# Kernel optimization log

Hardware: AMD Instinct MI355X
Metric: run time of the kernel (lower is better)

Reference implementation:

```python
import jax, jax.numpy as jnp
import numpy as np


def setup_inputs() -> dict:
    key = jax.random.key(0)
    k1, k2, k3 = jax.random.split(key, 3)
    B, C, H, W = 32, 768, 24, 24
    feat1 = jax.random.normal(k1, (B, C, H, W), dtype=jnp.float32)
    feat2 = jax.random.normal(k2, (B, C, H, W), dtype=jnp.float32)
    gamma = jax.random.normal(k3, (1,), dtype=jnp.float32)
    return {"feat1": feat1, "feat2": feat2, "gamma": gamma}


def reference(feat1, feat2, gamma):
    # CMA: channel-wise cross-modal attention over flattened spatial dim.
    B, C, H, W = feat1.shape
    q = feat1.reshape(B, C, H * W)          # [B, C, HW]
    kv = feat2.reshape(B, C, H * W)         # [B, C, HW] (k and v share this)
    attn = jnp.einsum('bcn,bdn->bcd', q, kv)          # [B, C, C] = q @ k^T
    attn = jax.nn.softmax(attn, axis=-1)
    info = jnp.einsum('bcd,bdn->bcn', attn, kv)       # [B, C, HW]
    info = info.reshape(B, C, H, W)
    return gamma[0] * info + feat1
```

## Files before the change

kernel.cpp:

```cpp
#include <hip/hip_runtime.h>

#define B_  32
#define C_  768
#define HW_ 576

#define NCQ 18
#define NCP 24

typedef _Float16 half8 __attribute__((ext_vector_type(8)));
typedef _Float16 half4 __attribute__((ext_vector_type(4)));
typedef float    f32x4 __attribute__((ext_vector_type(4)));

__device__ __forceinline__ void g2l16(const void* g, void* l) {
    __builtin_amdgcn_global_load_lds(
        (const __attribute__((address_space(1))) unsigned int*)g,
        (__attribute__((address_space(3))) unsigned int*)l, 16, 0, 0);
}

__device__ __forceinline__ int xcd_swz(int orig, int nwg) {
    int q = nwg >> 3, rr = nwg & 7;
    int xcd = orig & 7, idx = orig >> 3;
    int base = (xcd < rr) ? xcd * (q + 1) : rr * (q + 1) + (xcd - rr) * q;
    return base + idx;
}

__global__ __launch_bounds__(256) void prep_all(const float* __restrict__ f1,
                                                const float* __restrict__ f2,
                                                char* __restrict__ q16,
                                                char* __restrict__ kv16,
                                                char* __restrict__ vt,
                                                int b0, int nqk) {
    const int bid = blockIdx.x;
    if (bid < nqk) {
        int idx = bid * 256 + threadIdx.x;
        int x   = idx & 3;
        int row = (idx >> 2) & 127;
        int t3  = idx >> 9;
        int k0  = t3 % 18;
        int t4  = t3 / 18;
        int ti  = t4 % 6;
        int bz  = t4 / 6;
        int kc  = x ^ ((row >> 1) & 3);
        size_t src = ((size_t)(b0 + bz) * C_ + ti * 128 + row) * HW_ + k0 * 32 + kc * 8;
        f32x4 a0 = *(const f32x4*)(f1 + src);
        f32x4 a1 = *(const f32x4*)(f1 + src + 4);
        f32x4 c0 = *(const f32x4*)(f2 + src);
        f32x4 c1 = *(const f32x4*)(f2 + src + 4);
        half8 ha, hb;
        #pragma unroll
        for (int e = 0; e < 4; ++e) {
            ha[e] = (_Float16)a0[e]; ha[4 + e] = (_Float16)a1[e];
            hb[e] = (_Float16)c0[e]; hb[4 + e] = (_Float16)c1[e];
        }
        *(half8*)(q16  + (size_t)idx * 16) = ha;
        *(half8*)(kv16 + (size_t)idx * 16) = hb;
    } else {
        int idx = (bid - nqk) * 256 + threadIdx.x;
        int bz  = idx / 55296;
        int wl  = idx % 55296;
        int tj  = wl / 18432;
        int r   = wl % 18432;
        int k0  = r / 768;
        int r2  = r % 768;
        int n   = r2 >> 2;
        int x   = r2 & 3;
        int kc  = x ^ ((n >> 1) & 3);
        int c0  = k0 * 32 + kc * 8;
        const float* s = f2 + ((size_t)(b0 + bz) * C_ + c0) * HW_ + tj * 192 + n;
        half8 h;
        #pragma unroll
        for (int j = 0; j < 8; ++j) h[j] = (_Float16)s[(size_t)j * HW_];
        *(half8*)(vt + ((size_t)(bz * 3 + tj) * NCP + k0) * 12288 + n * 64 + x * 16) = h;
    }
}

__global__ __launch_bounds__(512, 4) void qk6(const char* __restrict__ q16,
                                              const char* __restrict__ kv16,
                                              float* __restrict__ attn,
                                              int nwg) {
    __shared__ __align__(16) char S[3][24576];
    const int wg = xcd_swz(blockIdx.x, nwg);
    const int bz = wg >> 4, rr0 = wg & 15, ti = rr0 >> 2, tj = rr0 & 3;
    const int t = threadIdx.x, lane = t & 63, w = t >> 6;
    const int rsub = lane >> 2, cb = (lane & 3) * 16;

    const char *p0, *p1, *p2;
    int o0, o1, o2;
    {
        auto arow = [&](int l) {
            int gr = ti * 192 + 16 * l + rsub;
            return q16 + ((size_t)(bz * 6 + (gr >> 7)) * NCQ) * 8192 + (gr & 127) * 64 + cb;
        };
        auto brow = [&](int l) {
            int gd = tj * 192 + 16 * l + rsub;
            return kv16 + ((size_t)(bz * 6 + (gd >> 7)) * NCQ) * 8192 + (gd & 127) * 64 + cb;
        };
        if (w < 4) {
            p0 = arow(2 * w);     o0 = (2 * w) * 1024;
            p1 = arow(2 * w + 1); o1 = (2 * w + 1) * 1024;
            p2 = brow(8 + w);     o2 = 12288 + (8 + w) * 1024;
        } else {
            int v = w - 4;
            p0 = brow(2 * v);     o0 = 12288 + (2 * v) * 1024;
            p1 = brow(2 * v + 1); o1 = 12288 + (2 * v + 1) * 1024;
            p2 = arow(8 + v);     o2 = (8 + v) * 1024;
        }
    }

    const int wr = (w >> 1) * 48, wc = (w & 1) * 96;
    const int r16 = lane & 15, cg = lane >> 4;
    int offA[3], offB[6];
    #pragma unroll
    for (int m = 0; m < 3; ++m) {
        int ra = wr + m * 16 + r16;
        offA[m] = ra * 64 + ((cg ^ ((ra >> 1) & 3)) << 4);
    }
    #pragma unroll
    for (int n = 0; n < 6; ++n) {
        int rb = wc + n * 16 + r16;
        offB[n] = 12288 + rb * 64 + ((cg ^ ((rb >> 1) & 3)) << 4);
    }

    f32x4 acc[3][6] = {};

#define STG(SLOT) do {                          \
        char* sb_ = &S[SLOT][0];                \
        g2l16(p0, sb_ + o0);                    \
        g2l16(p1, sb_ + o1);                    \
        g2l16(p2, sb_ + o2);                    \
        p0 += 8192; p1 += 8192; p2 += 8192;     \
    } while (0)

    STG(0); STG(1);
    int rd = 0, st = 2;
    for (int c = 0; c < NCQ; ++c) {
        if (c + 2 < NCQ) {
            STG(st); st = (st == 2) ? 0 : st + 1;
            asm volatile("s_waitcnt vmcnt(6)" ::: "memory");
        } else if (c + 2 == NCQ) {
            asm volatile("s_waitcnt vmcnt(3)" ::: "memory");
        } else {
            asm volatile("s_waitcnt vmcnt(0)" ::: "memory");
        }
        __builtin_amdgcn_s_barrier();
        const char* sb = &S[rd][0];
        rd = (rd == 2) ? 0 : rd + 1;
        half8 a0 = *(const half8*)(sb + offA[0]);
        half8 a1 = *(const half8*)(sb + offA[1]);
        half8 a2 = *(const half8*)(sb + offA[2]);
        __builtin_amdgcn_s_setprio(1);
        #pragma unroll
        for (int n = 0; n < 6; ++n) {
            half8 bn = *(const half8*)(sb + offB[n]);
            acc[0][n] = __builtin_amdgcn_mfma_f32_16x16x32_f16(a0, bn, acc[0][n], 0, 0, 0);
            acc[1][n] = __builtin_amdgcn_mfma_f32_16x16x32_f16(a1, bn, acc[1][n], 0, 0, 0);
            acc[2][n] = __builtin_amdgcn_mfma_f32_16x16x32_f16(a2, bn, acc[2][n], 0, 0, 0);
        }
        __builtin_amdgcn_s_setprio(0);
        __builtin_amdgcn_s_barrier();
    }
#undef STG

    float* ab = attn + ((size_t)bz * C_ + ti * 192) * C_ + tj * 192;
    const int col = lane & 15, rbase = (lane >> 4) * 4;
    #pragma unroll
    for (int m = 0; m < 3; ++m)
        #pragma unroll
        for (int n = 0; n < 6; ++n)
            #pragma unroll
            for (int rg = 0; rg < 4; ++rg)
                ab[(size_t)(wr + m * 16 + rbase + rg) * C_ + wc + n * 16 + col] = acc[m][n][rg];
}

__global__ __launch_bounds__(256) void softmax_p16(const float* __restrict__ attn,
                                                   char* __restrict__ p16,
                                                   const float* __restrict__ gamma) {
    const int R    = blockIdx.x * 4 + (threadIdx.x >> 6);
    const int lane = threadIdx.x & 63;
    const int bz   = R / C_;
    const int c    = R - bz * C_;
    const float* p = attn + (size_t)R * C_;

    f32x4 v[3];
    float mx = -1e30f;
    #pragma unroll
    for (int u = 0; u < 3; ++u) {
        v[u] = *(const f32x4*)(p + (size_t)(lane + 64 * u) * 4);
        #pragma unroll
        for (int e = 0; e < 4; ++e) mx = fmaxf(mx, v[u][e]);
    }
    #pragma unroll
    for (int o = 32; o > 0; o >>= 1) mx = fmaxf(mx, __shfl_xor(mx, o));

    float s = 0.f;
    #pragma unroll
    for (int u = 0; u < 3; ++u)
        #pragma unroll
        for (int e = 0; e < 4; ++e) {
            v[u][e] = __expf(v[u][e] - mx);
            s += v[u][e];
        }
    #pragma unroll
    for (int o = 32; o > 0; o >>= 1) s += __shfl_xor(s, o);
    const float scale = gamma[0] / s;

    const int sw = (c >> 1) & 3;
    char* tb = p16 + ((size_t)(bz * 6 + (c >> 7)) * NCP) * 8192;
    #pragma unroll
    for (int u = 0; u < 3; ++u) {
        int d0 = 4 * lane + 256 * u;
        int k0 = d0 >> 5;
        int x  = ((d0 >> 3) & 3) ^ sw;
        char* addr = tb + (size_t)k0 * 8192 + (c & 127) * 64 + x * 16 + (d0 & 7) * 2;
        half4 hv;
        #pragma unroll
        for (int e = 0; e < 4; ++e) hv[e] = (_Float16)(v[u][e] * scale);
        *(half4*)addr = hv;
    }
}

__global__ __launch_bounds__(512, 4) void pv6(const char* __restrict__ p16,
                                              const char* __restrict__ vt,
                                              const float* __restrict__ f1,
                                              float* __restrict__ out,
                                              int b0, int nwg) {
    __shared__ __align__(16) char S[3][24576];
    const int wg = xcd_swz(blockIdx.x, nwg);
    const int bz = wg / 12, rr0 = wg % 12, ti = rr0 / 3, tj = rr0 % 3;
    const int t = threadIdx.x, lane = t & 63, w = t >> 6;
    const int rsub = lane >> 2, cb = (lane & 3) * 16;

    const char *p0, *p1, *p2;
    int o0, o1, o2;
    long s0, s1, s2;
    {
        auto prow = [&](int l) {
            int gr = ti * 192 + 16 * l + rsub;
            return p16 + ((size_t)(bz * 6 + (gr >> 7)) * NCP) * 8192 + (gr & 127) * 64 + cb;
        };
        auto vrow = [&](int l) {
            int gn = 16 * l + rsub;
            return vt + ((size_t)(bz * 3 + tj) * NCP) * 12288 + gn * 64 + cb;
        };
        if (w < 4) {
            p0 = prow(2 * w);     o0 = (2 * w) * 1024;     s0 = 8192;
            p1 = prow(2 * w + 1); o1 = (2 * w + 1) * 1024; s1 = 8192;
            p2 = vrow(8 + w);     o2 = 12288 + (8 + w) * 1024; s2 = 12288;
        } else {
            int v = w - 4;
            p0 = vrow(2 * v);     o0 = 12288 + (2 * v) * 1024;     s0 = 12288;
            p1 = vrow(2 * v + 1); o1 = 12288 + (2 * v + 1) * 1024; s1 = 12288;
            p2 = prow(8 + v);     o2 = (8 + v) * 1024;             s2 = 8192;
        }
    }

    const int wr = (w >> 1) * 48, wc = (w & 1) * 96;
    const int r16 = lane & 15, cg = lane >> 4;
    int offA[3], offB[6];
    #pragma unroll
    for (int m = 0; m < 3; ++m) {
        int ra = wr + m * 16 + r16;
        offA[m] = ra * 64 + ((cg ^ ((ra >> 1) & 3)) << 4);
    }
    #pragma unroll
    for (int n = 0; n < 6; ++n) {
        int rb = wc + n * 16 + r16;
        offB[n] = 12288 + rb * 64 + ((cg ^ ((rb >> 1) & 3)) << 4);
    }

    f32x4 acc[3][6] = {};

#define STG(SLOT) do {                          \
        char* sb_ = &S[SLOT][0];                \
        g2l16(p0, sb_ + o0);                    \
        g2l16(p1, sb_ + o1);                    \
        g2l16(p2, sb_ + o2);                    \
        p0 += s0; p1 += s1; p2 += s2;           \
    } while (0)

    STG(0); STG(1);
    int rd = 0, st = 2;
    for (int c = 0; c < NCP; ++c) {
        if (c + 2 < NCP) {
            STG(st); st = (st == 2) ? 0 : st + 1;
            asm volatile("s_waitcnt vmcnt(6)" ::: "memory");
        } else if (c + 2 == NCP) {
            asm volatile("s_waitcnt vmcnt(3)" ::: "memory");
        } else {
            asm volatile("s_waitcnt vmcnt(0)" ::: "memory");
        }
        __builtin_amdgcn_s_barrier();
        const char* sb = &S[rd][0];
        rd = (rd == 2) ? 0 : rd + 1;
        half8 a0 = *(const half8*)(sb + offA[0]);
        half8 a1 = *(const half8*)(sb + offA[1]);
        half8 a2 = *(const half8*)(sb + offA[2]);
        __builtin_amdgcn_s_setprio(1);
        #pragma unroll
        for (int n = 0; n < 6; ++n) {
            half8 bn = *(const half8*)(sb + offB[n]);
            acc[0][n] = __builtin_amdgcn_mfma_f32_16x16x32_f16(a0, bn, acc[0][n], 0, 0, 0);
            acc[1][n] = __builtin_amdgcn_mfma_f32_16x16x32_f16(a1, bn, acc[1][n], 0, 0, 0);
            acc[2][n] = __builtin_amdgcn_mfma_f32_16x16x32_f16(a2, bn, acc[2][n], 0, 0, 0);
        }
        __builtin_amdgcn_s_setprio(0);
        __builtin_amdgcn_s_barrier();
    }
#undef STG

    const int b = b0 + bz;
    const float* f1b = f1 + ((size_t)b * C_ + ti * 192) * HW_ + tj * 192;
    float*       ob  = out + ((size_t)b * C_ + ti * 192) * HW_ + tj * 192;
    const int col = lane & 15, rbase = (lane >> 4) * 4;
    #pragma unroll
    for (int m = 0; m < 3; ++m)
        #pragma unroll
        for (int n = 0; n < 6; ++n)
            #pragma unroll
            for (int rg = 0; rg < 4; ++rg) {
                int r2 = wr + m * 16 + rbase + rg;
                int c2 = wc + n * 16 + col;
                ob[(size_t)r2 * HW_ + c2] = acc[m][n][rg] + f1b[(size_t)r2 * HW_ + c2];
            }
}

extern "C" void kernel_launch(void* const* d_in, const int* in_sizes, int n_in,
                              void* d_out, int out_size, void* d_ws, size_t ws_size,
                              hipStream_t stream) {
    const float* feat1 = (const float*)d_in[0];
    const float* feat2 = (const float*)d_in[1];
    const float* gamma = (const float*)d_in[2];
    float* out = (float*)d_out;

    const size_t SZ_Q    = (size_t)C_ * HW_ * 2;
    const size_t SZ_ATTN = (size_t)C_ * C_  * 4;
    const size_t SZ_P    = (size_t)C_ * C_  * 2;
    const size_t per_batch = SZ_ATTN + 3 * SZ_Q + SZ_P;

    int nb = (int)(ws_size / per_batch);
    if (nb < 1) nb = 1;
    if (nb > B_) nb = B_;

    char* ws    = (char*)d_ws;
    float* attn = (float*)ws;
    char* q16   = ws + (size_t)nb * SZ_ATTN;
    char* kv16  = q16 + (size_t)nb * SZ_Q;
    char* vtb   = kv16 + (size_t)nb * SZ_Q;
    char* p16   = vtb + (size_t)nb * SZ_Q;

    for (int b0 = 0; b0 < B_; b0 += nb) {
        int cur = (B_ - b0 < nb) ? (B_ - b0) : nb;
        prep_all<<<cur * 432, 256, 0, stream>>>(feat1, feat2, q16, kv16, vtb, b0, cur * 216);
        qk6<<<cur * 16, 512, 0, stream>>>(q16, kv16, attn, cur * 16);
        softmax_p16<<<cur * 192, 256, 0, stream>>>(attn, p16, gamma);
        pv6<<<cur * 12, 512, 0, stream>>>(p16, vtb, feat1, out, b0, cur * 12);
    }
}
```

Baseline: 146.5 us.

## Transpose V via shared memory and retile PV into 128x192 double-buffered tiles

The V-transpose part of prep now stages a 32x192 fp32 tile in padded shared memory, so global reads are coalesced float4 loads instead of strided scalar reads. Each block now handles one tile, which cuts the grid for that part. The PV kernel changes from 512-thread 192x192 tiles with triple buffering to 256-thread 128x192 tiles with double buffering, giving more workgroups (18 per batch) and higher occupancy. The trade-offs are shallower prefetch and more B-tile reloads across row tiles.

```diff
diff --git a/kernel.cpp b/kernel.cpp
--- a/kernel.cpp
+++ b/kernel.cpp
@@ -30,6 +30,7 @@
                                                 char* __restrict__ kv16,
                                                 char* __restrict__ vt,
                                                 int b0, int nqk) {
+    __shared__ float Vsh[32 * 201];
     const int bid = blockIdx.x;
     if (bid < nqk) {
         int idx = bid * 256 + threadIdx.x;
@@ -55,22 +56,30 @@
         *(half8*)(q16  + (size_t)idx * 16) = ha;
         *(half8*)(kv16 + (size_t)idx * 16) = hb;
     } else {
-        int idx = (bid - nqk) * 256 + threadIdx.x;
-        int bz  = idx / 55296;
-        int wl  = idx % 55296;
-        int tj  = wl / 18432;
-        int r   = wl % 18432;
-        int k0  = r / 768;
-        int r2  = r % 768;
-        int n   = r2 >> 2;
-        int x   = r2 & 3;
-        int kc  = x ^ ((n >> 1) & 3);
-        int c0  = k0 * 32 + kc * 8;
-        const float* s = f2 + ((size_t)(b0 + bz) * C_ + c0) * HW_ + tj * 192 + n;
-        half8 h;
-        #pragma unroll
-        for (int j = 0; j < 8; ++j) h[j] = (_Float16)s[(size_t)j * HW_];
-        *(half8*)(vt + ((size_t)(bz * 3 + tj) * NCP + k0) * 12288 + n * 64 + x * 16) = h;
+        int bid2 = bid - nqk;
+        int bz = bid2 / 72, rem = bid2 % 72, k0 = rem / 3, tj = rem % 3;
+        int b  = b0 + bz;
+        int t  = threadIdx.x;
+        #pragma unroll
+        for (int p = 0; p < 6; ++p) {
+            int fidx = p * 256 + t;
+            int dd = fidx / 48, c4 = fidx % 48;
+            f32x4 v = *(const f32x4*)(f2 + ((size_t)b * C_ + k0 * 32 + dd) * HW_ + tj * 192 + c4 * 4);
+            #pragma unroll
+            for (int e = 0; e < 4; ++e) Vsh[dd * 201 + c4 * 4 + e] = v[e];
+        }
+        __syncthreads();
+        char* ob = vt + ((size_t)(bz * 3 + tj) * NCP + k0) * 12288;
+        #pragma unroll
+        for (int p = 0; p < 3; ++p) {
+            int o = p * 256 + t;
+            int x = o & 3, n = o >> 2;
+            int kc = x ^ ((n >> 1) & 3);
+            half8 h;
+            #pragma unroll
+            for (int j = 0; j < 8; ++j) h[j] = (_Float16)Vsh[(kc * 8 + j) * 201 + n];
+            *(half8*)(ob + o * 16) = h;
+        }
     }
 }
 
@@ -219,106 +228,112 @@
     }
 }
 
-__global__ __launch_bounds__(512, 4) void pv6(const char* __restrict__ p16,
+__global__ __launch_bounds__(256, 8) void pv7(const char* __restrict__ p16,
                                               const char* __restrict__ vt,
                                               const float* __restrict__ f1,
                                               float* __restrict__ out,
                                               int b0, int nwg) {
-    __shared__ __align__(16) char S[3][24576];
+    __shared__ __align__(16) char S[2][20480];
     const int wg = xcd_swz(blockIdx.x, nwg);
-    const int bz = wg / 12, rr0 = wg % 12, ti = rr0 / 3, tj = rr0 % 3;
+    const int bz = wg / 18, rem = wg % 18, ti = rem / 3, tj = rem % 3;
     const int t = threadIdx.x, lane = t & 63, w = t >> 6;
     const int rsub = lane >> 2, cb = (lane & 3) * 16;
 
-    const char *p0, *p1, *p2;
-    int o0, o1, o2;
-    long s0, s1, s2;
-    {
-        auto prow = [&](int l) {
-            int gr = ti * 192 + 16 * l + rsub;
-            return p16 + ((size_t)(bz * 6 + (gr >> 7)) * NCP) * 8192 + (gr & 127) * 64 + cb;
-        };
-        auto vrow = [&](int l) {
-            int gn = 16 * l + rsub;
-            return vt + ((size_t)(bz * 3 + tj) * NCP) * 12288 + gn * 64 + cb;
-        };
-        if (w < 4) {
-            p0 = prow(2 * w);     o0 = (2 * w) * 1024;     s0 = 8192;
-            p1 = prow(2 * w + 1); o1 = (2 * w + 1) * 1024; s1 = 8192;
-            p2 = vrow(8 + w);     o2 = 12288 + (8 + w) * 1024; s2 = 12288;
-        } else {
-            int v = w - 4;
-            p0 = vrow(2 * v);     o0 = 12288 + (2 * v) * 1024;     s0 = 12288;
-            p1 = vrow(2 * v + 1); o1 = 12288 + (2 * v + 1) * 1024; s1 = 12288;
-            p2 = prow(8 + v);     o2 = (8 + v) * 1024;             s2 = 8192;
-        }
-    }
-
-    const int wr = (w >> 1) * 48, wc = (w & 1) * 96;
+    const char* Ab = p16 + ((size_t)(bz * 6 + ti) * NCP) * 8192  + rsub * 64 + cb;
+    const char* Bb = vt  + ((size_t)(bz * 3 + tj) * NCP) * 12288 + rsub * 64 + cb;
+
+    const char *p0, *p1, *p2, *p3, *p4;
+    int o0, o1, o2, o3, o4;
+    long s0, s1, s2, s3, s4;
+    if (w == 0) {
+        p0 = Ab;          o0 = 0;          s0 = 8192;
+        p1 = Ab + 1024;   o1 = 1024;       s1 = 8192;
+        p2 = Ab + 2048;   o2 = 2048;       s2 = 8192;
+        p3 = Ab + 3072;   o3 = 3072;       s3 = 8192;
+        p4 = Ab + 4096;   o4 = 4096;       s4 = 8192;
+    } else if (w == 1) {
+        p0 = Ab + 5120;   o0 = 5120;       s0 = 8192;
+        p1 = Ab + 6144;   o1 = 6144;       s1 = 8192;
+        p2 = Ab + 7168;   o2 = 7168;       s2 = 8192;
+        p3 = Bb;          o3 = 8192;       s3 = 12288;
+        p4 = Bb + 1024;   o4 = 9216;       s4 = 12288;
+    } else if (w == 2) {
+        p0 = Bb + 2048;   o0 = 10240;      s0 = 12288;
+        p1 = Bb + 3072;   o1 = 11264;      s1 = 12288;
+        p2 = Bb + 4096;   o2 = 12288;      s2 = 12288;
+        p3 = Bb + 5120;   o3 = 13312;      s3 = 12288;
+        p4 = Bb + 6144;   o4 = 14336;      s4 = 12288;
+    } else {
+        p0 = Bb + 7168;   o0 = 15360;      s0 = 12288;
+        p1 = Bb + 8192;   o1 = 16384;      s1 = 12288;
+        p2 = Bb + 9216;   o2 = 17408;      s2 = 12288;
+        p3 = Bb + 10240;  o3 = 18432;      s3 = 12288;
+        p4 = Bb + 11264;  o4 = 19456;      s4 = 12288;
+    }
+
+    const int wc = w * 48;
     const int r16 = lane & 15, cg = lane >> 4;
-    int offA[3], offB[6];
-    #pragma unroll
-    for (int m = 0; m < 3; ++m) {
-        int ra = wr + m * 16 + r16;
+    int offA[8], offB[3];
+    #pragma unroll
+    for (int m = 0; m < 8; ++m) {
+        int ra = m * 16 + r16;
         offA[m] = ra * 64 + ((cg ^ ((ra >> 1) & 3)) << 4);
     }
     #pragma unroll
-    for (int n = 0; n < 6; ++n) {
+    for (int n = 0; n < 3; ++n) {
         int rb = wc + n * 16 + r16;
-        offB[n] = 12288 + rb * 64 + ((cg ^ ((rb >> 1) & 3)) << 4);
-    }
-
-    f32x4 acc[3][6] = {};
+        offB[n] = 8192 + rb * 64 + ((cg ^ ((rb >> 1) & 3)) << 4);
+    }
+
+    f32x4 acc[8][3] = {};
 
 #define STG(SLOT) do {                          \
         char* sb_ = &S[SLOT][0];                \
-        g2l16(p0, sb_ + o0);                    \
-        g2l16(p1, sb_ + o1);                    \
-        g2l16(p2, sb_ + o2);                    \
-        p0 += s0; p1 += s1; p2 += s2;           \
+        g2l16(p0, sb_ + o0); p0 += s0;          \
+        g2l16(p1, sb_ + o1); p1 += s1;          \
+        g2l16(p2, sb_ + o2); p2 += s2;          \
+        g2l16(p3, sb_ + o3); p3 += s3;          \
+        g2l16(p4, sb_ + o4); p4 += s4;          \
     } while (0)
 
-    STG(0); STG(1);
-    int rd = 0, st = 2;
+    STG(0);
     for (int c = 0; c < NCP; ++c) {
-        if (c + 2 < NCP) {
-            STG(st); st = (st == 2) ? 0 : st + 1;
-            asm volatile("s_waitcnt vmcnt(6)" ::: "memory");
-        } else if (c + 2 == NCP) {
-            asm volatile("s_waitcnt vmcnt(3)" ::: "memory");
+        const int cur = c & 1;
+        if (c + 1 < NCP) {
+            STG(cur ^ 1);
+            asm volatile("s_waitcnt vmcnt(5)" ::: "memory");
         } else {
             asm volatile("s_waitcnt vmcnt(0)" ::: "memory");
         }
         __builtin_amdgcn_s_barrier();
-        const char* sb = &S[rd][0];
-        rd = (rd == 2) ? 0 : rd + 1;
-        half8 a0 = *(const half8*)(sb + offA[0]);
-        half8 a1 = *(const half8*)(sb + offA[1]);
-        half8 a2 = *(const half8*)(sb + offA[2]);
+        const char* sb = &S[cur][0];
+        half8 a[8], bb8[3];
+        #pragma unroll
+        for (int m = 0; m < 8; ++m) a[m]  = *(const half8*)(sb + offA[m]);
+        #pragma unroll
+        for (int n = 0; n < 3; ++n) bb8[n] = *(const half8*)(sb + offB[n]);
         __builtin_amdgcn_s_setprio(1);
         #pragma unroll
-        for (int n = 0; n < 6; ++n) {
-            half8 bn = *(const half8*)(sb + offB[n]);
-            acc[0][n] = __builtin_amdgcn_mfma_f32_16x16x32_f16(a0, bn, acc[0][n], 0, 0, 0);
-            acc[1][n] = __builtin_amdgcn_mfma_f32_16x16x32_f16(a1, bn, acc[1][n], 0, 0, 0);
-            acc[2][n] = __builtin_amdgcn_mfma_f32_16x16x32_f16(a2, bn, acc[2][n], 0, 0, 0);
-        }
+        for (int m = 0; m < 8; ++m)
+            #pragma unroll
+            for (int n = 0; n < 3; ++n)
+                acc[m][n] = __builtin_amdgcn_mfma_f32_16x16x32_f16(a[m], bb8[n], acc[m][n], 0, 0, 0);
         __builtin_amdgcn_s_setprio(0);
         __builtin_amdgcn_s_barrier();
     }
 #undef STG
 
     const int b = b0 + bz;
-    const float* f1b = f1 + ((size_t)b * C_ + ti * 192) * HW_ + tj * 192;
-    float*       ob  = out + ((size_t)b * C_ + ti * 192) * HW_ + tj * 192;
+    const float* f1b = f1 + ((size_t)b * C_ + ti * 128) * HW_ + tj * 192;
+    float*       ob  = out + ((size_t)b * C_ + ti * 128) * HW_ + tj * 192;
     const int col = lane & 15, rbase = (lane >> 4) * 4;
     #pragma unroll
-    for (int m = 0; m < 3; ++m)
-        #pragma unroll
-        for (int n = 0; n < 6; ++n)
+    for (int m = 0; m < 8; ++m)
+        #pragma unroll
+        for (int n = 0; n < 3; ++n)
             #pragma unroll
             for (int rg = 0; rg < 4; ++rg) {
-                int r2 = wr + m * 16 + rbase + rg;
+                int r2 = m * 16 + rbase + rg;
                 int c2 = wc + n * 16 + col;
                 ob[(size_t)r2 * HW_ + c2] = acc[m][n][rg] + f1b[(size_t)r2 * HW_ + c2];
             }
@@ -350,9 +365,9 @@
 
     for (int b0 = 0; b0 < B_; b0 += nb) {
         int cur = (B_ - b0 < nb) ? (B_ - b0) : nb;
-        prep_all<<<cur * 432, 256, 0, stream>>>(feat1, feat2, q16, kv16, vtb, b0, cur * 216);
+        prep_all<<<cur * 288, 256, 0, stream>>>(feat1, feat2, q16, kv16, vtb, b0, cur * 216);
         qk6<<<cur * 16, 512, 0, stream>>>(q16, kv16, attn, cur * 16);
         softmax_p16<<<cur * 192, 256, 0, stream>>>(attn, p16, gamma);
-        pv6<<<cur * 12, 512, 0, stream>>>(p16, vtb, feat1, out, b0, cur * 12);
-    }
-}
+        pv7<<<cur * 18, 256, 0, stream>>>(p16, vtb, feat1, out, b0, cur * 18);
+    }
+}
```

Result: slower. 216.4 us (+47.7%).
